# Optimization experiments

Measured on AMD Instinct MI355X. Metric: run time of the kernel, lower is better.

The kernel has to match this reference:

```python
import jax, jax.numpy as jnp
import numpy as np

NUM_CAPSULE = 5
DIM_CAPSULE = 5
ROUTINGS = 4
T_EPSILON = 1e-07


def squash(x, axis=-1):
    # Note: this module's 'squash' is pure norm-normalization (no v^2/(1+v^2) factor)
    s_squared_norm = jnp.sum(x * x, axis=axis, keepdims=True)
    return x / jnp.sqrt(s_squared_norm + T_EPSILON)


def setup_inputs() -> dict:
    key = jax.random.key(0)
    k1, k2 = jax.random.split(key)
    batch, seq, d_in = 1024, 512, 120
    x = jax.random.normal(k1, (batch, seq, d_in), dtype=jnp.float32)
    # xavier_normal for fan_in=120, fan_out=25
    std = float(np.sqrt(2.0 / (d_in + NUM_CAPSULE * DIM_CAPSULE)))
    W = jax.random.normal(k2, (1, d_in, NUM_CAPSULE * DIM_CAPSULE), dtype=jnp.float32) * std
    return {"x": x, "W": W}


def reference(x, W):
    batch, inp, _ = x.shape
    # u_hat_vecs: [batch, num_capsule, input_num_capsule, dim_capsule]
    u_hat = jnp.matmul(x, W[0])  # [b, inp, 25]
    u_hat = u_hat.reshape(batch, inp, NUM_CAPSULE, DIM_CAPSULE).transpose(0, 2, 1, 3)
    b = jnp.zeros((batch, NUM_CAPSULE, inp), dtype=u_hat.dtype)
    outputs = None
    for i in range(ROUTINGS):
        # torch code softmaxes over the num_capsule axis (dim 1 of b)
        c = jax.nn.softmax(b, axis=1)  # [b, ncaps, inp]
        outputs = squash(jnp.einsum('bij,bijk->bik', c, u_hat))  # [b, ncaps, dcap]
        if i < ROUTINGS - 1:
            b = jnp.einsum('bik,bijk->bij', outputs, u_hat)
    return outputs
```

## Files before the change

### kernel.cpp

```cpp
#include <hip/hip_runtime.h>


#define NCAP 5
#define DCAP 5
#define NOUT 25
#define DIN 120
#define SEQ 512
#define ROUTINGS 4

__global__ __launch_bounds__(256) void caps_kernel(
    const float* __restrict__ x,
    const float* __restrict__ W,
    float* __restrict__ out)
{
    const int b    = blockIdx.x;
    const int t    = threadIdx.x;
    const int lane = t & 63;
    const int wv   = t >> 6;

    __shared__ float red[4][NOUT];

    float acc[2][NOUT];
#pragma unroll
    for (int r = 0; r < 2; ++r)
#pragma unroll
        for (int j = 0; j < NOUT; ++j) acc[r][j] = 0.f;

    const float* xb = x + (size_t)b * SEQ * DIN;
#pragma unroll
    for (int r = 0; r < 2; ++r) {
        const float4* xp = (const float4*)(xb + (2 * t + r) * DIN);
        for (int u = 0; u < DIN / 4; ++u) {
            float4 v = xp[u];
            const float* wr = W + u * 4 * NOUT;
#pragma unroll
            for (int j = 0; j < NOUT; ++j) {
                float a = acc[r][j];
                a = fmaf(v.x, wr[j],          a);
                a = fmaf(v.y, wr[j + NOUT],   a);
                a = fmaf(v.z, wr[j + 2*NOUT], a);
                a = fmaf(v.w, wr[j + 3*NOUT], a);
                acc[r][j] = a;
            }
        }
    }

    float bb[2][NCAP];
#pragma unroll
    for (int r = 0; r < 2; ++r)
#pragma unroll
        for (int c = 0; c < NCAP; ++c) bb[r][c] = 0.f;

    float o[NOUT];

    for (int it = 0; it < ROUTINGS; ++it) {
        float p[NOUT];
#pragma unroll
        for (int j = 0; j < NOUT; ++j) p[j] = 0.f;

#pragma unroll
        for (int r = 0; r < 2; ++r) {
            float m = bb[r][0];
#pragma unroll
            for (int c = 1; c < NCAP; ++c) m = fmaxf(m, bb[r][c]);
            float e[NCAP]; float se = 0.f;
#pragma unroll
            for (int c = 0; c < NCAP; ++c) { e[c] = __expf(bb[r][c] - m); se += e[c]; }
            float inv = 1.f / se;
#pragma unroll
            for (int c = 0; c < NCAP; ++c) {
                float cc = e[c] * inv;
#pragma unroll
                for (int k = 0; k < DCAP; ++k)
                    p[c*DCAP + k] = fmaf(cc, acc[r][c*DCAP + k], p[c*DCAP + k]);
            }
        }

#pragma unroll
        for (int d = 1; d < 64; d <<= 1)
#pragma unroll
            for (int j = 0; j < NOUT; ++j) p[j] += __shfl_xor(p[j], d, 64);

        if (lane == 0) {
#pragma unroll
            for (int j = 0; j < NOUT; ++j) red[wv][j] = p[j];
        }
        __syncthreads();
        float s[NOUT];
#pragma unroll
        for (int j = 0; j < NOUT; ++j)
            s[j] = red[0][j] + red[1][j] + red[2][j] + red[3][j];
        __syncthreads();

#pragma unroll
        for (int c = 0; c < NCAP; ++c) {
            float ss = 0.f;
#pragma unroll
            for (int k = 0; k < DCAP; ++k)
                ss = fmaf(s[c*DCAP + k], s[c*DCAP + k], ss);
            float sc = rsqrtf(ss + 1e-7f);
#pragma unroll
            for (int k = 0; k < DCAP; ++k) o[c*DCAP + k] = s[c*DCAP + k] * sc;
        }

        if (it < ROUTINGS - 1) {
#pragma unroll
            for (int r = 0; r < 2; ++r)
#pragma unroll
                for (int c = 0; c < NCAP; ++c) {
                    float d0 = 0.f;
#pragma unroll
                    for (int k = 0; k < DCAP; ++k)
                        d0 = fmaf(o[c*DCAP + k], acc[r][c*DCAP + k], d0);
                    bb[r][c] = d0;
                }
        }
    }

    if (t < NOUT) out[(size_t)b * NOUT + t] = o[t];
}

extern "C" void kernel_launch(void* const* d_in, const int* in_sizes, int n_in,
                              void* d_out, int out_size, void* d_ws, size_t ws_size,
                              hipStream_t stream) {
    const float* x   = (const float*)d_in[0];
    const float* W   = (const float*)d_in[1];
    float*       o   = (float*)d_out;
    const int batch  = in_sizes[0] / (SEQ * DIN);
    caps_kernel<<<dim3(batch), dim3(256), 0, stream>>>(x, W, o);
}
```

Before: 433.0 us.

## Stage x through padded LDS tiles for coalesced loads and shared W reads

Before, each thread read its own two rows of x with strided float4 loads, so accesses across a wavefront were uncoalesced. The kernel now loads x in K-tiles of 24 columns, cooperatively and coalesced, into a padded shared-memory buffer. Each thread then reads its two rows from LDS and processes both rows in the same inner loop, so each W element is loaded once and used for two rows. This adds about 53KB of LDS per block and two barriers per tile, which may reduce occupancy.

After: 401.5 us. 7.3% less time.

```diff
diff --git a/kernel.cpp b/kernel.cpp
--- a/kernel.cpp
+++ b/kernel.cpp
@@ -7,6 +7,9 @@
 #define DIN 120
 #define SEQ 512
 #define ROUTINGS 4
+
+#define KT   24
+#define PAD  26
 
 __global__ __launch_bounds__(256) void caps_kernel(
     const float* __restrict__ x,
@@ -18,7 +21,10 @@
     const int lane = t & 63;
     const int wv   = t >> 6;
 
+    __shared__ float xt[SEQ * PAD];
     __shared__ float red[4][NOUT];
+
+    const float* xb = x + (size_t)b * SEQ * DIN;
 
     float acc[2][NOUT];
 #pragma unroll
@@ -26,23 +32,42 @@
 #pragma unroll
         for (int j = 0; j < NOUT; ++j) acc[r][j] = 0.f;
 
-    const float* xb = x + (size_t)b * SEQ * DIN;
+    const int r0 = (2 * t) * PAD;
+    const int r1 = (2 * t + 1) * PAD;
+
+    for (int tile = 0; tile < 5; ++tile) {
+        const int k0 = tile * KT;
+
 #pragma unroll
-    for (int r = 0; r < 2; ++r) {
-        const float4* xp = (const float4*)(xb + (2 * t + r) * DIN);
-        for (int u = 0; u < DIN / 4; ++u) {
-            float4 v = xp[u];
-            const float* wr = W + u * 4 * NOUT;
+        for (int i = 0; i < 12; ++i) {
+            int f   = t + 256 * i;
+            int row = f / 6;
+            int q   = f - row * 6;
+            float4 v = *(const float4*)(xb + row * DIN + k0 + 4 * q);
+            float* dst = &xt[row * PAD + 4 * q];
+            *(float2*)(dst)     = make_float2(v.x, v.y);
+            *(float2*)(dst + 2) = make_float2(v.z, v.w);
+        }
+        __syncthreads();
+
+#pragma unroll
+        for (int u = 0; u < 6; ++u) {
+            float2 a0 = *(const float2*)&xt[r0 + 4 * u];
+            float2 a1 = *(const float2*)&xt[r0 + 4 * u + 2];
+            float2 b0 = *(const float2*)&xt[r1 + 4 * u];
+            float2 b1 = *(const float2*)&xt[r1 + 4 * u + 2];
+            const float* wr = W + (k0 + 4 * u) * NOUT;
 #pragma unroll
             for (int j = 0; j < NOUT; ++j) {
-                float a = acc[r][j];
-                a = fmaf(v.x, wr[j],          a);
-                a = fmaf(v.y, wr[j + NOUT],   a);
-                a = fmaf(v.z, wr[j + 2*NOUT], a);
-                a = fmaf(v.w, wr[j + 3*NOUT], a);
-                acc[r][j] = a;
+                float w0 = wr[j];
+                float w1 = wr[j + NOUT];
+                float w2 = wr[j + 2 * NOUT];
+                float w3 = wr[j + 3 * NOUT];
+                acc[0][j] = fmaf(a1.y, w3, fmaf(a1.x, w2, fmaf(a0.y, w1, fmaf(a0.x, w0, acc[0][j]))));
+                acc[1][j] = fmaf(b1.y, w3, fmaf(b1.x, w2, fmaf(b0.y, w1, fmaf(b0.x, w0, acc[1][j]))));
             }
         }
+        __syncthreads();
     }
 
     float bb[2][NCAP];
```

## Split capsule layer into tiled LDS GEMM kernel and separate routing kernel

Applied to the files above, without the earlier changes.

Replaces the single fused kernel, where each thread read two strided x rows straight from global memory, with two kernels. A GEMM kernel stages 64-row tiles of x in padded, double-buffered LDS with register prefetch, splits the K and output dimensions across waves, and writes u_hat to workspace. A routing kernel then loads each batch's u_hat into LDS and runs the unchanged routing loop. The aim is coalesced x loads with latency overlap, in exchange for an extra global round trip of u_hat and a second launch.

Measured after the change: 404.2 us. -6.7%, faster.

```diff
diff --git a/kernel.cpp b/kernel.cpp
--- a/kernel.cpp
+++ b/kernel.cpp
@@ -8,41 +8,130 @@
 #define SEQ 512
 #define ROUTINGS 4
 
-__global__ __launch_bounds__(256) void caps_kernel(
+#define TROWS 64
+#define TILES 8
+#define XS   121
+#define NF4  1920
+
+__global__ __launch_bounds__(256) void gemm_kernel(
     const float* __restrict__ x,
     const float* __restrict__ W,
+    float* __restrict__ u)
+{
+    __shared__ __align__(16) float xs[2][TROWS * XS];
+    __shared__ __align__(16) float us[2][TROWS * NOUT];
+
+    const int t    = threadIdx.x;
+    const int lane = t & 63;
+    const int wv   = __builtin_amdgcn_readfirstlane(t >> 6);
+    const int jh   = wv & 1;
+    const int kh   = wv >> 1;
+    const int j0   = jh * 12;
+    const int jcnt = jh ? 13 : 12;
+
+    const long rowsBase = (long)blockIdx.x * (TILES * TROWS);
+
+    {
+        const float4* src = (const float4*)(x + rowsBase * DIN);
+#pragma unroll
+        for (int i = 0; i < 8; ++i) {
+            int f = t + 256 * i;
+            if (f < NF4) {
+                float4 v = src[f];
+                int r = f / 30, q = f - 30 * r;
+                float* d = &xs[0][r * XS + 4 * q];
+                d[0] = v.x; d[1] = v.y; d[2] = v.z; d[3] = v.w;
+            }
+        }
+    }
+    __syncthreads();
+
+    for (int tile = 0; tile < TILES; ++tile) {
+        const int cur  = tile & 1;
+        const int nxt  = cur ^ 1;
+        const bool more = (tile + 1 < TILES);
+
+        float4 L[8];
+        if (more) {
+            const float4* src =
+                (const float4*)(x + (rowsBase + (long)(tile + 1) * TROWS) * DIN);
+#pragma unroll
+            for (int i = 0; i < 8; ++i) {
+                int f = t + 256 * i;
+                L[i] = (f < NF4) ? src[f] : make_float4(0.f, 0.f, 0.f, 0.f);
+            }
+        }
+
+        float acc[13];
+#pragma unroll
+        for (int j = 0; j < 13; ++j) acc[j] = 0.f;
+        const float* xr = &xs[cur][lane * XS + kh * 60];
+        const float* wk = W + (kh * 60) * NOUT + j0;
+#pragma unroll 4
+        for (int k = 0; k < 60; ++k) {
+            float xv = xr[k];
+            const float* wr = wk + k * NOUT;
+#pragma unroll
+            for (int j = 0; j < 13; ++j) acc[j] = fmaf(xv, wr[j], acc[j]);
+        }
+
+        float* ur = &us[cur][lane * NOUT + j0];
+        if (kh == 0) {
+            for (int j = 0; j < jcnt; ++j) ur[j] = acc[j];
+        }
+        __syncthreads();
+        if (kh == 1) {
+            for (int j = 0; j < jcnt; ++j) ur[j] += acc[j];
+        }
+        if (more) {
+#pragma unroll
+            for (int i = 0; i < 8; ++i) {
+                int f = t + 256 * i;
+                if (f < NF4) {
+                    int r = f / 30, q = f - 30 * r;
+                    float* d = &xs[nxt][r * XS + 4 * q];
+                    d[0] = L[i].x; d[1] = L[i].y; d[2] = L[i].z; d[3] = L[i].w;
+                }
+            }
+        }
+        __syncthreads();
+
+        const float4* s4 = (const float4*)&us[cur][0];
+        float4* d4 = (float4*)(u + (rowsBase + (long)tile * TROWS) * NOUT);
+#pragma unroll
+        for (int i = 0; i < 2; ++i) {
+            int f = t + 256 * i;
+            if (f < TROWS * NOUT / 4) d4[f] = s4[f];
+        }
+    }
+}
+
+__global__ __launch_bounds__(256) void route_kernel(
+    const float* __restrict__ u,
     float* __restrict__ out)
 {
-    const int b    = blockIdx.x;
+    __shared__ __align__(16) float usm[SEQ * NOUT];
+    __shared__ float red[4][NOUT];
+
     const int t    = threadIdx.x;
     const int lane = t & 63;
     const int wv   = t >> 6;
 
-    __shared__ float red[4][NOUT];
-
-    float acc[2][NOUT];
-#pragma unroll
-    for (int r = 0; r < 2; ++r)
-#pragma unroll
-        for (int j = 0; j < NOUT; ++j) acc[r][j] = 0.f;
-
-    const float* xb = x + (size_t)b * SEQ * DIN;
+    const float4* src = (const float4*)(u + (size_t)blockIdx.x * SEQ * NOUT);
+    float4* d4 = (float4*)usm;
+#pragma unroll
+    for (int i = 0; i < 13; ++i) {
+        int f = t + 256 * i;
+        if (f < SEQ * NOUT / 4) d4[f] = src[f];
+    }
+    __syncthreads();
+
+    float uh[2][NOUT];
 #pragma unroll
     for (int r = 0; r < 2; ++r) {
-        const float4* xp = (const float4*)(xb + (2 * t + r) * DIN);
-        for (int u = 0; u < DIN / 4; ++u) {
-            float4 v = xp[u];
-            const float* wr = W + u * 4 * NOUT;
-#pragma unroll
-            for (int j = 0; j < NOUT; ++j) {
-                float a = acc[r][j];
-                a = fmaf(v.x, wr[j],          a);
-                a = fmaf(v.y, wr[j + NOUT],   a);
-                a = fmaf(v.z, wr[j + 2*NOUT], a);
-                a = fmaf(v.w, wr[j + 3*NOUT], a);
-                acc[r][j] = a;
-            }
-        }
+        const float* rr = &usm[(t + 256 * r) * NOUT];
+#pragma unroll
+        for (int j = 0; j < NOUT; ++j) uh[r][j] = rr[j];
     }
 
     float bb[2][NCAP];
@@ -72,7 +161,7 @@
                 float cc = e[c] * inv;
 #pragma unroll
                 for (int k = 0; k < DCAP; ++k)
-                    p[c*DCAP + k] = fmaf(cc, acc[r][c*DCAP + k], p[c*DCAP + k]);
+                    p[c*DCAP + k] = fmaf(cc, uh[r][c*DCAP + k], p[c*DCAP + k]);
             }
         }
 
@@ -111,21 +200,26 @@
                     float d0 = 0.f;
 #pragma unroll
                     for (int k = 0; k < DCAP; ++k)
-                        d0 = fmaf(o[c*DCAP + k], acc[r][c*DCAP + k], d0);
+                        d0 = fmaf(o[c*DCAP + k], uh[r][c*DCAP + k], d0);
                     bb[r][c] = d0;
                 }
         }
     }
 
-    if (t < NOUT) out[(size_t)b * NOUT + t] = o[t];
+    if (t < NOUT) out[(size_t)blockIdx.x * NOUT + t] = o[t];
 }
 
 extern "C" void kernel_launch(void* const* d_in, const int* in_sizes, int n_in,
                               void* d_out, int out_size, void* d_ws, size_t ws_size,
                               hipStream_t stream) {
-    const float* x   = (const float*)d_in[0];
-    const float* W   = (const float*)d_in[1];
-    float*       o   = (float*)d_out;
-    const int batch  = in_sizes[0] / (SEQ * DIN);
-    caps_kernel<<<dim3(batch), dim3(256), 0, stream>>>(x, W, o);
+    const float* x = (const float*)d_in[0];
+    const float* W = (const float*)d_in[1];
+    float* out     = (float*)d_out;
+    float* u       = (float*)d_ws;
+
+    const int nrows = in_sizes[0] / DIN;
+    const int batch = nrows / SEQ;
+
+    gemm_kernel <<<dim3(nrows / (TILES * TROWS)), dim3(256), 0, stream>>>(x, W, u);
+    route_kernel<<<dim3(batch),                   dim3(256), 0, stream>>>(u, out);
 }
```
